# Kernel optimization log

Hardware: AMD Instinct MI355X
Metric: run time of the kernel (lower is better)

The kernel has to match this reference:

```python
import jax, jax.numpy as jnp
import numpy as np

N, D, E, H, TOPK = 16384, 1024, 8, 4096, 2


def setup_inputs() -> dict:
    key = jax.random.key(0)
    ks = jax.random.split(key, 7)
    s_in = 1.0 / np.sqrt(D)
    s_h = 1.0 / np.sqrt(H)
    return {
        "x": jax.random.normal(ks[0], (N, D), jnp.float32),
        "Wg": jax.random.uniform(ks[1], (D, E), jnp.float32, -s_in, s_in),
        "bg": jnp.zeros((E,), jnp.float32),
        "W1": jax.random.uniform(ks[2], (E, D, H), jnp.float32, -s_in, s_in),
        "b1": jax.random.uniform(ks[3], (E, H), jnp.float32, -s_in, s_in),
        "W2": jax.random.uniform(ks[4], (E, H, D), jnp.float32, -s_h, s_h),
        "b2": jax.random.uniform(ks[5], (E, D), jnp.float32, -s_h, s_h),
    }


def _moe_forward(x, Wg, bg, W1, b1, W2, b2):
    # Gate: softmax over experts, top-k, renormalize (standard TopKGate)
    logits = x @ Wg + bg                       # (N, E)
    probs = jax.nn.softmax(logits, axis=-1)
    gates, idxs = jax.lax.top_k(probs, TOPK)   # (N, K)
    gates = gates / jnp.sum(gates, axis=-1, keepdims=True)

    # combine weight per token per expert: cw[n,e] = sum_k gates[n,k]*[idxs[n,k]==e]
    onehot = jax.nn.one_hot(idxs, E, dtype=x.dtype)        # (N, K, E)
    cw = jnp.einsum("nk,nke->ne", gates, onehot)           # (N, E)

    # per-expert 2-layer MLP, gated combine (loop over small fixed expert set)
    out = jnp.zeros_like(x)
    for e in range(E):
        h = jax.nn.relu(x @ W1[e] + b1[e])     # (N, H)
        y = h @ W2[e] + b2[e]                  # (N, D)
        out = out + cw[:, e:e + 1] * y

    # aux loss: for each expert with >=1 routed token, add mean(gates[:,0])^2
    counts = jnp.sum(onehot, axis=(0, 1))                  # (E,)
    active = (counts > 0).astype(x.dtype)                  # (E,)
    m = jnp.mean(gates[:, 0])
    aux_loss = jnp.sum(active) * m * m
    return out, aux_loss


def reference(x, Wg, bg, W1, b1, W2, b2):
    return _moe_forward(x, Wg, bg, W1, b1, W2, b2)
```

## Files before the change

kernel.cpp:

```cpp
#include <hip/hip_runtime.h>
#include <stdint.h>

typedef unsigned short u16;
typedef __bf16 bf16x8 __attribute__((ext_vector_type(8)));
typedef float f32x4 __attribute__((ext_vector_type(4)));

#define N_TOK 16384
#define DIM   1024
#define NEXP  8
#define HID   4096
#define MTILES 264
#define PADROWS 33792

__device__ __forceinline__ u16 f2bf(float f) {
  uint32_t u = __builtin_bit_cast(uint32_t, f);
  u += 0x7fffu + ((u >> 16) & 1u);
  return (u16)(u >> 16);
}

__device__ __forceinline__ float bf2f(u16 v) {
  uint32_t u = (uint32_t)v << 16;
  return __builtin_bit_cast(float, u);
}

__device__ __forceinline__ void gload16(const void* g, void* l) {
  __builtin_amdgcn_global_load_lds(
      (const __attribute__((address_space(1))) uint32_t*)g,
      (__attribute__((address_space(3))) uint32_t*)l, 16, 0, 0);
}


__global__ void k_zero(int* counts) {
  if (threadIdx.x < NEXP) counts[threadIdx.x] = 0;
}

__global__ void k_tcast(const float* __restrict__ src, u16* __restrict__ dst,
                        int R, int C) {
  __shared__ float tile[32][33];
  int nc = C >> 5, nr = R >> 5;
  int t = blockIdx.x;
  int cb = t % nc; t /= nc;
  int rb = t % nr; int ee = t / nr;
  const float* s0 = src + ((size_t)ee * R + (size_t)rb * 32) * C + cb * 32;
  int tx = threadIdx.x & 31, ty = threadIdx.x >> 5;
#pragma unroll
  for (int i = 0; i < 4; ++i)
    tile[ty + i * 8][tx] = s0[(size_t)(ty + i * 8) * C + tx];
  __syncthreads();
  u16* d0 = dst + ((size_t)ee * C + (size_t)cb * 32) * R + rb * 32;
#pragma unroll
  for (int i = 0; i < 4; ++i)
    d0[(size_t)(ty + i * 8) * R + tx] = f2bf(tile[tx][ty + i * 8]);
}


__global__ __launch_bounds__(256) void k_gate(
    const float* __restrict__ x, const float* __restrict__ Wg,
    const float* __restrict__ bg, u16* __restrict__ xb,
    int* __restrict__ tok_e, float* __restrict__ tok_g,
    float* __restrict__ blocksums) {
  __shared__ float wg_s[NEXP * DIM];
  __shared__ float s4[4];
  for (int i = threadIdx.x; i < NEXP * DIM; i += 256) {
    int k = i >> 3, e = i & 7;
    wg_s[e * DIM + k] = Wg[i];
  }
  __syncthreads();
  int lane = threadIdx.x & 63, wv = threadIdx.x >> 6;
  int n = blockIdx.x * 4 + wv;
  const float4* xr4 = (const float4*)(x + (size_t)n * DIM);
  float4 xv[4];
#pragma unroll
  for (int i = 0; i < 4; ++i) xv[i] = xr4[lane + 64 * i];
  ushort4* xo4 = (ushort4*)(xb + (size_t)n * DIM);
#pragma unroll
  for (int i = 0; i < 4; ++i) {
    ushort4 p;
    p.x = f2bf(xv[i].x); p.y = f2bf(xv[i].y);
    p.z = f2bf(xv[i].z); p.w = f2bf(xv[i].w);
    xo4[lane + 64 * i] = p;
  }
  float acc[8];
#pragma unroll
  for (int e = 0; e < 8; ++e) {
    const float4* w4 = (const float4*)(wg_s + e * DIM);
    float a = 0.f;
#pragma unroll
    for (int i = 0; i < 4; ++i) {
      float4 wv4 = w4[lane + 64 * i];
      a += xv[i].x * wv4.x + xv[i].y * wv4.y + xv[i].z * wv4.z +
           xv[i].w * wv4.w;
    }
    acc[e] = a;
  }
#pragma unroll
  for (int e = 0; e < 8; ++e)
#pragma unroll
    for (int off = 32; off > 0; off >>= 1)
      acc[e] += __shfl_xor(acc[e], off);

  if (lane == 0) {
    float l0 = -1e30f, l1 = -1e30f; int e0 = 0, e1 = 0;
#pragma unroll
    for (int e = 0; e < 8; ++e) {
      float v = acc[e] + bg[e];
      if (v > l0) { l1 = l0; e1 = e0; l0 = v; e0 = e; }
      else if (v > l1) { l1 = v; e1 = e; }
    }
    float g0 = 1.f / (1.f + expf(l1 - l0));
    float g1 = 1.f - g0;
    tok_e[2 * n] = e0; tok_e[2 * n + 1] = e1;
    tok_g[2 * n] = g0; tok_g[2 * n + 1] = g1;
    s4[wv] = g0;
  }
  __syncthreads();
  if (threadIdx.x == 0) blocksums[blockIdx.x] = s4[0] + s4[1] + s4[2] + s4[3];
}


__global__ __launch_bounds__(256) void k_hist(const int* __restrict__ tok_e,
                                              int* __restrict__ counts) {
  __shared__ int lcnt[8];
  if (threadIdx.x < 8) lcnt[threadIdx.x] = 0;
  __syncthreads();
  int base4 = (blockIdx.x * 256 + threadIdx.x) * 2;
  const int4* t4 = (const int4*)tok_e;
  int4 a = t4[base4], b = t4[base4 + 1];
  int v[8] = {a.x, a.y, a.z, a.w, b.x, b.y, b.z, b.w};
  int c[8];
#pragma unroll
  for (int ee = 0; ee < 8; ++ee) {
    int s = 0;
#pragma unroll
    for (int i = 0; i < 8; ++i) s += (v[i] == ee);
    c[ee] = s;
  }
  int lane = threadIdx.x & 63;
#pragma unroll
  for (int ee = 0; ee < 8; ++ee) {
    int s = c[ee];
#pragma unroll
    for (int off = 32; off > 0; off >>= 1) s += __shfl_xor(s, off);
    if (lane == 0 && s) atomicAdd(&lcnt[ee], s);
  }
  __syncthreads();
  if (threadIdx.x < 8 && lcnt[threadIdx.x])
    atomicAdd(&counts[threadIdx.x], lcnt[threadIdx.x]);
}


__global__ __launch_bounds__(256) void k_setup(
    const int* __restrict__ counts, const float* __restrict__ blocksums,
    int* __restrict__ padded_off, int* __restrict__ cursor,
    int* __restrict__ row2tok, float* __restrict__ aux_out) {
  __shared__ float red[256];
  __shared__ int off_s[9];
  float s = 0.f;
  for (int i = threadIdx.x; i < 4096; i += 256) s += blocksums[i];
  red[threadIdx.x] = s;
  __syncthreads();
  for (int st = 128; st > 0; st >>= 1) {
    if (threadIdx.x < st) red[threadIdx.x] += red[threadIdx.x + st];
    __syncthreads();
  }
  if (threadIdx.x == 0) {
    int off = 0, nact = 0;
    for (int e = 0; e < 8; ++e) {
      off_s[e] = off;
      int c = counts[e];
      if (c > 0) nact++;
      off += ((c + 127) >> 7) << 7;
      cursor[e] = 0;
    }
    off_s[8] = off;
    for (int e = 0; e <= 8; ++e) padded_off[e] = off_s[e];
    float m = red[0] / (float)N_TOK;
    *aux_out = (float)nact * m * m;
  }
  __syncthreads();
  for (int idx = threadIdx.x; idx < NEXP * 128; idx += 256) {
    int e = idx >> 7, i = idx & 127;
    int slot = off_s[e] + counts[e] + i;
    if (slot < off_s[e + 1]) row2tok[slot] = 0;
  }
}


__global__ __launch_bounds__(256) void k_scatter(
    int* __restrict__ tok_e, const int* __restrict__ padded_off,
    int* __restrict__ cursor, int* __restrict__ row2tok) {
  __shared__ int lcnt[8], lbase[8];
  if (threadIdx.x < 8) lcnt[threadIdx.x] = 0;
  __syncthreads();
  int n = blockIdx.x * 256 + threadIdx.x;
  int e0 = tok_e[2 * n], e1 = tok_e[2 * n + 1];
  int p0 = atomicAdd(&lcnt[e0], 1);
  int p1 = atomicAdd(&lcnt[e1], 1);
  __syncthreads();
  if (threadIdx.x < 8 && lcnt[threadIdx.x])
    lbase[threadIdx.x] = atomicAdd(&cursor[threadIdx.x], lcnt[threadIdx.x]);
  __syncthreads();
  int s0 = padded_off[e0] + lbase[e0] + p0;
  int s1 = padded_off[e1] + lbase[e1] + p1;
  row2tok[s0] = n;
  row2tok[s1] = n;
  tok_e[2 * n] = s0;
  tok_e[2 * n + 1] = s1;
}


template <int KDIM, int MODE, int NTL>
__global__ __launch_bounds__(256, 3) void k_gemm(
    const u16* __restrict__ Asrc, const u16* __restrict__ Wt,
    const float* __restrict__ bias, const int* __restrict__ row2tok,
    const int* __restrict__ padded_off, u16* __restrict__ Out) {
  __shared__ u16 Abuf[3][4096];
  __shared__ u16 Bbuf[3][4096];
  constexpr int NDIM = MODE ? DIM : HID;
  static_assert((1 << NTL) == NDIM / 128, "NT must equal n-tile count");
  int d = blockIdx.x;
  int xcd = d & 7;
  int n_t = (d >> 3) & ((1 << NTL) - 1);
  int rg  = d >> (3 + NTL);
  int row0 = (rg * 8 + xcd) * 128;
  if (row0 >= padded_off[8]) return;
  int e = 0;
  while (row0 >= padded_off[e + 1]) ++e;
  int n0 = n_t * 128;
  int tid = threadIdx.x, lane = tid & 63, wv = tid >> 6;
  int wm = wv >> 1, wn = wv & 1;
  int fr = lane & 15, fq = lane >> 4;
  int ra0 = tid >> 2, ra1 = 64 + (tid >> 2);
  int ca = (((tid & 3) ^ ((tid >> 3) & 3))) * 8;
  const u16 *asrc0, *asrc1;
  if (MODE == 0) {
    asrc0 = Asrc + (size_t)row2tok[row0 + ra0] * KDIM + ca;
    asrc1 = Asrc + (size_t)row2tok[row0 + ra1] * KDIM + ca;
  } else {
    asrc0 = Asrc + (size_t)(row0 + ra0) * KDIM + ca;
    asrc1 = Asrc + (size_t)(row0 + ra1) * KDIM + ca;
  }
  const u16* bb = Wt + (size_t)e * (HID * DIM);
  const u16* bsrc0 = bb + (size_t)(n0 + ra0) * KDIM + ca;
  const u16* bsrc1 = bb + (size_t)(n0 + ra1) * KDIM + ca;
  int lo = wv * 512;
  int sq = (fq ^ ((fr >> 1) & 3)) * 8;

  f32x4 acc[4][4];
#pragma unroll
  for (int i = 0; i < 4; ++i)
#pragma unroll
    for (int j = 0; j < 4; ++j) acc[i][j] = (f32x4){0.f, 0.f, 0.f, 0.f};
  bf16x8 av[4], bv[4];

#define STG(b, kt)                                 \
  do {                                             \
    int ko = (kt) * 32;                            \
    gload16(asrc0 + ko, &Abuf[b][lo]);             \
    gload16(asrc1 + ko, &Abuf[b][2048 + lo]);      \
    gload16(bsrc0 + ko, &Bbuf[b][lo]);             \
    gload16(bsrc1 + ko, &Bbuf[b][2048 + lo]);      \
  } while (0)

#define CMP(b)                                                                 \
  do {                                                                         \
    _Pragma("unroll") for (int fm = 0; fm < 4; ++fm)                           \
        av[fm] = *(const bf16x8*)&Abuf[b][(wm * 64 + fm * 16 + fr) * 32 + sq]; \
    _Pragma("unroll") for (int fn = 0; fn < 4; ++fn)                           \
        bv[fn] = *(const bf16x8*)&Bbuf[b][(wn * 64 + fn * 16 + fr) * 32 + sq]; \
    _Pragma("unroll") for (int fm = 0; fm < 4; ++fm)                           \
        _Pragma("unroll") for (int fn = 0; fn < 4; ++fn)                       \
            acc[fm][fn] = __builtin_amdgcn_mfma_f32_16x16x32_bf16(             \
                av[fm], bv[fn], acc[fm][fn], 0, 0, 0);                         \
  } while (0)

  constexpr int NK = KDIM / 32;
  STG(0, 0);
  STG(1, 1);
  int rb = 0;
  for (int kt = 0; kt < NK - 2; ++kt) {
    int sb = rb + 2; if (sb >= 3) sb -= 3;
    STG(sb, kt + 2);
    asm volatile("s_waitcnt vmcnt(8)" ::: "memory");
    asm volatile("s_barrier" ::: "memory");
    CMP(rb);
    asm volatile("s_waitcnt lgkmcnt(0)" ::: "memory");
    asm volatile("s_barrier" ::: "memory");
    if (++rb == 3) rb = 0;
  }
  asm volatile("s_waitcnt vmcnt(4)" ::: "memory");
  asm volatile("s_barrier" ::: "memory");
  CMP(rb);
  if (++rb == 3) rb = 0;
  asm volatile("s_waitcnt vmcnt(0)" ::: "memory");
  asm volatile("s_barrier" ::: "memory");
  CMP(rb);
#undef STG
#undef CMP

  float bv4[4];
#pragma unroll
  for (int fn = 0; fn < 4; ++fn)
    bv4[fn] = bias[e * NDIM + n0 + wn * 64 + fn * 16 + fr];

#pragma unroll
  for (int fm = 0; fm < 4; ++fm) {
#pragma unroll
    for (int j = 0; j < 4; ++j) {
      int grow = row0 + wm * 64 + fm * 16 + fq * 4 + j;
      u16* orow = Out + (size_t)grow * NDIM + n0 + wn * 64 + fr;
#pragma unroll
      for (int fn = 0; fn < 4; ++fn) {
        float v = acc[fm][fn][j] + bv4[fn];
        if (MODE == 0) v = v > 0.f ? v : 0.f;
        orow[fn * 16] = f2bf(v);
      }
    }
  }
}


__global__ __launch_bounds__(256) void k_combine(
    const u16* __restrict__ y, const int* __restrict__ slots,
    const float* __restrict__ tok_g, float* __restrict__ out) {
  int n = blockIdx.x;
  int s0 = slots[2 * n], s1 = slots[2 * n + 1];
  float g0 = tok_g[2 * n], g1 = tok_g[2 * n + 1];
  int d = threadIdx.x * 4;
  ushort4 a = *(const ushort4*)(y + (size_t)s0 * DIM + d);
  ushort4 b = *(const ushort4*)(y + (size_t)s1 * DIM + d);
  float4 o;
  o.x = g0 * bf2f(a.x) + g1 * bf2f(b.x);
  o.y = g0 * bf2f(a.y) + g1 * bf2f(b.y);
  o.z = g0 * bf2f(a.z) + g1 * bf2f(b.z);
  o.w = g0 * bf2f(a.w) + g1 * bf2f(b.w);
  *(float4*)(out + (size_t)n * DIM + d) = o;
}


extern "C" void kernel_launch(void* const* d_in, const int* in_sizes, int n_in,
                              void* d_out, int out_size, void* d_ws,
                              size_t ws_size, hipStream_t stream) {
  const float* x  = (const float*)d_in[0];
  const float* Wg = (const float*)d_in[1];
  const float* bg = (const float*)d_in[2];
  const float* W1 = (const float*)d_in[3];
  const float* b1 = (const float*)d_in[4];
  const float* W2 = (const float*)d_in[5];
  const float* b2 = (const float*)d_in[6];
  float* out = (float*)d_out;

  char* w = (char*)d_ws;
  u16* xb          = (u16*)(w);
  u16* y           = (u16*)(w);
  u16* w1t         = (u16*)(w + 33554432);
  u16* w2t         = (u16*)(w + 100663296);
  u16* h           = (u16*)(w + 167772160);
  int* tok_e       = (int*)(w + 444596224);
  float* tok_g     = (float*)(w + 444727296);
  int* counts      = (int*)(w + 444858368);
  int* cursor      = (int*)(w + 444858624);
  int* padded_off  = (int*)(w + 444858880);
  int* row2tok     = (int*)(w + 444859136);
  float* blocksums = (float*)(w + 445129472);

  k_zero<<<1, 64, 0, stream>>>(counts);
  k_gate<<<4096, 256, 0, stream>>>(x, Wg, bg, xb, tok_e, tok_g, blocksums);
  k_hist<<<16, 256, 0, stream>>>(tok_e, counts);
  k_setup<<<1, 256, 0, stream>>>(counts, blocksums, padded_off, cursor, row2tok,
                                 out + (size_t)N_TOK * DIM);
  k_scatter<<<64, 256, 0, stream>>>(tok_e, padded_off, cursor, row2tok);
  k_tcast<<<32768, 256, 0, stream>>>(W1, w1t, DIM, HID);
  k_tcast<<<32768, 256, 0, stream>>>(W2, w2t, HID, DIM);
  k_gemm<DIM, 0, 5><<<MTILES * (HID / 128), 256, 0, stream>>>(
      xb, w1t, b1, row2tok, padded_off, h);
  k_gemm<HID, 1, 3><<<MTILES * (DIM / 128), 256, 0, stream>>>(
      h, w2t, b2, row2tok, padded_off, y);
  k_combine<<<N_TOK, 256, 0, stream>>>(y, tok_e, tok_g, out);
}
```

Before: 874.9 us.

## Use 256x256 tiles with 8-wave pipelined schedule for first expert GEMM

Replaces the first expert GEMM with a 512-thread kernel computing 256x256 output tiles, using large LDS buffers with an 8-phase interleaved load/compute schedule, raised wave priority around MFMA bursts, and per-expert padding to 256 rows. This targets higher arithmetic intensity and better overlap of global-to-LDS loads with matrix math in the largest GEMM. The workspace is reorganised so one transposed weight buffer is reused between the two GEMMs, with the output y split across two regions. Larger padding adds wasted rows and the big tile cuts occupancy, and the reordered transposes serialize weight casts with GEMMs.

After: 827.0 us. -5.5%, faster.

```diff
diff --git a/kernel.cpp b/kernel.cpp
--- a/kernel.cpp
+++ b/kernel.cpp
@@ -9,8 +9,9 @@
 #define DIM   1024
 #define NEXP  8
 #define HID   4096
-#define MTILES 264
-#define PADROWS 33792
+#define MT256 136
+#define MT128 272
+#define PADROWS 34816
 
 __device__ __forceinline__ u16 f2bf(float f) {
   uint32_t u = __builtin_bit_cast(uint32_t, f);
@@ -169,7 +170,7 @@
       off_s[e] = off;
       int c = counts[e];
       if (c > 0) nact++;
-      off += ((c + 127) >> 7) << 7;
+      off += ((c + 255) >> 8) << 8;
       cursor[e] = 0;
     }
     off_s[8] = off;
@@ -178,8 +179,8 @@
     *aux_out = (float)nact * m * m;
   }
   __syncthreads();
-  for (int idx = threadIdx.x; idx < NEXP * 128; idx += 256) {
-    int e = idx >> 7, i = idx & 127;
+  for (int idx = threadIdx.x; idx < NEXP * 256; idx += 256) {
+    int e = idx >> 8, i = idx & 255;
     int slot = off_s[e] + counts[e] + i;
     if (slot < off_s[e + 1]) row2tok[slot] = 0;
   }
@@ -209,19 +210,139 @@
 }
 
 
-template <int KDIM, int MODE, int NTL>
-__global__ __launch_bounds__(256, 3) void k_gemm(
-    const u16* __restrict__ Asrc, const u16* __restrict__ Wt,
-    const float* __restrict__ bias, const int* __restrict__ row2tok,
-    const int* __restrict__ padded_off, u16* __restrict__ Out) {
+__global__ __launch_bounds__(512, 2) void k_gemm1_8p(
+    const u16* __restrict__ xb, const u16* __restrict__ w1t,
+    const float* __restrict__ b1, const int* __restrict__ row2tok,
+    const int* __restrict__ padded_off, u16* __restrict__ h) {
+  __shared__ u16 ldsA[32768];
+  __shared__ u16 ldsB[32768];
+  int n0 = blockIdx.x * 256;
+  int row0 = blockIdx.y * 256;
+  if (row0 >= padded_off[8]) return;
+  int e = 0;
+  while (row0 >= padded_off[e + 1]) ++e;
+  int tid = threadIdx.x, lane = tid & 63, wv = tid >> 6;
+  int wm = wv >> 2, wn = wv & 3;
+  int fr = lane & 15, fq = lane >> 4;
+  int r = tid >> 2;
+  int clog = ((tid & 3) ^ ((tid >> 3) & 3)) * 8;
+  const u16* a0 = xb + (size_t)row2tok[row0 + r] * DIM + clog;
+  const u16* a1 = xb + (size_t)row2tok[row0 + 128 + r] * DIM + clog;
+  const u16* wp = w1t + (size_t)e * (HID * DIM);
+  const u16* b0p = wp + (size_t)(n0 + r) * DIM + clog;
+  const u16* b1p = wp + (size_t)(n0 + 128 + r) * DIM + clog;
+
+  f32x4 acc[8][4];
+#pragma unroll
+  for (int i = 0; i < 8; ++i)
+#pragma unroll
+    for (int j = 0; j < 4; ++j) acc[i][j] = (f32x4){0.f, 0.f, 0.f, 0.f};
+  bf16x8 av[4], bv[4];
+
+#define ST1(ISB, T, KK, KOF)                                              \
+  do {                                                                   \
+    u16* d_ = ((ISB) ? ldsB : ldsA) + ((T) * 2 + (KK)) * 8192 + wv * 512; \
+    gload16(((ISB) ? b0p : a0) + (KOF), d_);                             \
+    gload16(((ISB) ? b1p : a1) + (KOF), d_ + 4096);                      \
+  } while (0)
+
+#define RD8(T, KK, IH, LB)                                                \
+  do {                                                                   \
+    const u16* Ar = ldsA + ((T) * 2 + (KK)) * 8192;                      \
+    _Pragma("unroll") for (int i = 0; i < 4; ++i) {                      \
+      int ar = wm * 128 + ((IH) * 4 + i) * 16 + fr;                      \
+      av[i] = *(const bf16x8*)&Ar[ar * 32 + ((fq ^ ((ar >> 1) & 3)) * 8)]; \
+    }                                                                    \
+    if (LB) {                                                            \
+      const u16* Br = ldsB + ((T) * 2 + (KK)) * 8192;                    \
+      _Pragma("unroll") for (int j = 0; j < 4; ++j) {                    \
+        int br = wn * 64 + j * 16 + fr;                                  \
+        bv[j] = *(const bf16x8*)&Br[br * 32 + ((fq ^ ((br >> 1) & 3)) * 8)]; \
+      }                                                                  \
+    }                                                                    \
+  } while (0)
+
+#define PH(T, KK, IH, LB, DOST, SB, STT, SKK, SKOF, VM6, VM0)            \
+  do {                                                                   \
+    RD8(T, KK, IH, LB);                                                  \
+    if (DOST) ST1(SB, STT, SKK, SKOF);                                   \
+    if (VM6) asm volatile("s_waitcnt vmcnt(6)" ::: "memory");            \
+    if (VM0) asm volatile("s_waitcnt vmcnt(0)" ::: "memory");            \
+    asm volatile("s_barrier" ::: "memory");                              \
+    asm volatile("s_waitcnt lgkmcnt(0)" ::: "memory");                   \
+    __builtin_amdgcn_sched_barrier(0);                                   \
+    __builtin_amdgcn_s_setprio(1);                                       \
+    _Pragma("unroll") for (int i = 0; i < 4; ++i)                        \
+      _Pragma("unroll") for (int j = 0; j < 4; ++j)                      \
+        acc[(IH) * 4 + i][j] = __builtin_amdgcn_mfma_f32_16x16x32_bf16(  \
+            av[i], bv[j], acc[(IH) * 4 + i][j], 0, 0, 0);                \
+    __builtin_amdgcn_s_setprio(0);                                       \
+    asm volatile("s_barrier" ::: "memory");                              \
+  } while (0)
+
+  ST1(1, 0, 0, 0);  ST1(0, 0, 0, 0);  ST1(1, 0, 1, 32); ST1(0, 0, 1, 32);
+  ST1(1, 1, 0, 64); ST1(0, 1, 0, 64); ST1(1, 1, 1, 96);
+  asm volatile("s_waitcnt vmcnt(6)" ::: "memory");
+  asm volatile("s_barrier" ::: "memory");
+
+  constexpr int NI = DIM / 128;
+  for (int kt = 0; kt < NI - 1; ++kt) {
+    int k0 = kt * 128;
+    PH(0, 0, 0, 1, 1, 0, 1, 1, k0 + 96,  0, 0);
+    PH(0, 0, 1, 0, 1, 1, 0, 0, k0 + 128, 0, 0);
+    PH(0, 1, 0, 1, 1, 0, 0, 0, k0 + 128, 0, 0);
+    PH(0, 1, 1, 0, 1, 1, 0, 1, k0 + 160, 1, 0);
+    PH(1, 0, 0, 1, 1, 0, 0, 1, k0 + 160, 0, 0);
+    PH(1, 0, 1, 0, 1, 1, 1, 0, k0 + 192, 0, 0);
+    PH(1, 1, 0, 1, 1, 0, 1, 0, k0 + 192, 0, 0);
+    PH(1, 1, 1, 0, 1, 1, 1, 1, k0 + 224, 1, 0);
+  }
+  {
+    int k0 = (NI - 1) * 128;
+    PH(0, 0, 0, 1, 1, 0, 1, 1, k0 + 96, 0, 0);
+    PH(0, 0, 1, 0, 0, 0, 0, 0, 0, 0, 0);
+    PH(0, 1, 0, 1, 0, 0, 0, 0, 0, 0, 0);
+    PH(0, 1, 1, 0, 0, 0, 0, 0, 0, 0, 1);
+    PH(1, 0, 0, 1, 0, 0, 0, 0, 0, 0, 0);
+    PH(1, 0, 1, 0, 0, 0, 0, 0, 0, 0, 0);
+    PH(1, 1, 0, 1, 0, 0, 0, 0, 0, 0, 0);
+    PH(1, 1, 1, 0, 0, 0, 0, 0, 0, 0, 0);
+  }
+#undef PH
+#undef RD8
+#undef ST1
+
+  float bv4[4];
+#pragma unroll
+  for (int j = 0; j < 4; ++j)
+    bv4[j] = b1[e * HID + n0 + wn * 64 + j * 16 + fr];
+
+#pragma unroll
+  for (int rf = 0; rf < 8; ++rf) {
+#pragma unroll
+    for (int jj = 0; jj < 4; ++jj) {
+      int grow = row0 + wm * 128 + rf * 16 + fq * 4 + jj;
+      u16* hr = h + (size_t)grow * HID + n0 + wn * 64 + fr;
+#pragma unroll
+      for (int j = 0; j < 4; ++j) {
+        float v = acc[rf][j][jj] + bv4[j];
+        hr[j * 16] = f2bf(v > 0.f ? v : 0.f);
+      }
+    }
+  }
+}
+
+
+__global__ __launch_bounds__(256, 3) void k_gemm2(
+    const u16* __restrict__ hh, const u16* __restrict__ w2t,
+    const float* __restrict__ b2, const int* __restrict__ padded_off,
+    u16* __restrict__ y0, u16* __restrict__ y1) {
   __shared__ u16 Abuf[3][4096];
   __shared__ u16 Bbuf[3][4096];
-  constexpr int NDIM = MODE ? DIM : HID;
-  static_assert((1 << NTL) == NDIM / 128, "NT must equal n-tile count");
   int d = blockIdx.x;
   int xcd = d & 7;
-  int n_t = (d >> 3) & ((1 << NTL) - 1);
-  int rg  = d >> (3 + NTL);
+  int n_t = (d >> 3) & 7;
+  int rg  = d >> 6;
   int row0 = (rg * 8 + xcd) * 128;
   if (row0 >= padded_off[8]) return;
   int e = 0;
@@ -232,17 +353,11 @@
   int fr = lane & 15, fq = lane >> 4;
   int ra0 = tid >> 2, ra1 = 64 + (tid >> 2);
   int ca = (((tid & 3) ^ ((tid >> 3) & 3))) * 8;
-  const u16 *asrc0, *asrc1;
-  if (MODE == 0) {
-    asrc0 = Asrc + (size_t)row2tok[row0 + ra0] * KDIM + ca;
-    asrc1 = Asrc + (size_t)row2tok[row0 + ra1] * KDIM + ca;
-  } else {
-    asrc0 = Asrc + (size_t)(row0 + ra0) * KDIM + ca;
-    asrc1 = Asrc + (size_t)(row0 + ra1) * KDIM + ca;
-  }
-  const u16* bb = Wt + (size_t)e * (HID * DIM);
-  const u16* bsrc0 = bb + (size_t)(n0 + ra0) * KDIM + ca;
-  const u16* bsrc1 = bb + (size_t)(n0 + ra1) * KDIM + ca;
+  const u16* asrc0 = hh + (size_t)(row0 + ra0) * HID + ca;
+  const u16* asrc1 = hh + (size_t)(row0 + ra1) * HID + ca;
+  const u16* bb = w2t + (size_t)e * (HID * DIM);
+  const u16* bsrc0 = bb + (size_t)(n0 + ra0) * HID + ca;
+  const u16* bsrc1 = bb + (size_t)(n0 + ra1) * HID + ca;
   int lo = wv * 512;
   int sq = (fq ^ ((fr >> 1) & 3)) * 8;
 
@@ -274,7 +389,7 @@
                 av[fm], bv[fn], acc[fm][fn], 0, 0, 0);                         \
   } while (0)
 
-  constexpr int NK = KDIM / 32;
+  constexpr int NK = HID / 32;
   STG(0, 0);
   STG(1, 1);
   int rb = 0;
@@ -301,34 +416,38 @@
   float bv4[4];
 #pragma unroll
   for (int fn = 0; fn < 4; ++fn)
-    bv4[fn] = bias[e * NDIM + n0 + wn * 64 + fn * 16 + fr];
+    bv4[fn] = b2[e * DIM + n0 + wn * 64 + fn * 16 + fr];
 
 #pragma unroll
   for (int fm = 0; fm < 4; ++fm) {
 #pragma unroll
     for (int j = 0; j < 4; ++j) {
       int grow = row0 + wm * 64 + fm * 16 + fq * 4 + j;
-      u16* orow = Out + (size_t)grow * NDIM + n0 + wn * 64 + fr;
-#pragma unroll
-      for (int fn = 0; fn < 4; ++fn) {
-        float v = acc[fm][fn][j] + bv4[fn];
-        if (MODE == 0) v = v > 0.f ? v : 0.f;
-        orow[fn * 16] = f2bf(v);
-      }
+      u16* ybase = grow < 16384 ? y0 + (size_t)grow * DIM
+                                : y1 + (size_t)(grow - 16384) * DIM;
+      u16* orow = ybase + n0 + wn * 64 + fr;
+#pragma unroll
+      for (int fn = 0; fn < 4; ++fn)
+        orow[fn * 16] = f2bf(acc[fm][fn][j] + bv4[fn]);
     }
   }
 }
 
 
 __global__ __launch_bounds__(256) void k_combine(
-    const u16* __restrict__ y, const int* __restrict__ slots,
-    const float* __restrict__ tok_g, float* __restrict__ out) {
+    const u16* __restrict__ y0, const u16* __restrict__ y1,
+    const int* __restrict__ slots, const float* __restrict__ tok_g,
+    float* __restrict__ out) {
   int n = blockIdx.x;
   int s0 = slots[2 * n], s1 = slots[2 * n + 1];
   float g0 = tok_g[2 * n], g1 = tok_g[2 * n + 1];
   int d = threadIdx.x * 4;
-  ushort4 a = *(const ushort4*)(y + (size_t)s0 * DIM + d);
-  ushort4 b = *(const ushort4*)(y + (size_t)s1 * DIM + d);
+  const u16* ya = (s0 < 16384 ? y0 + (size_t)s0 * DIM
+                              : y1 + (size_t)(s0 - 16384) * DIM) + d;
+  const u16* yb = (s1 < 16384 ? y0 + (size_t)s1 * DIM
+                              : y1 + (size_t)(s1 - 16384) * DIM) + d;
+  ushort4 a = *(const ushort4*)ya;
+  ushort4 b = *(const ushort4*)yb;
   float4 o;
   o.x = g0 * bf2f(a.x) + g1 * bf2f(b.x);
   o.y = g0 * bf2f(a.y) + g1 * bf2f(b.y);
@@ -352,17 +471,17 @@
 
   char* w = (char*)d_ws;
   u16* xb          = (u16*)(w);
-  u16* y           = (u16*)(w);
-  u16* w1t         = (u16*)(w + 33554432);
-  u16* w2t         = (u16*)(w + 100663296);
-  u16* h           = (u16*)(w + 167772160);
-  int* tok_e       = (int*)(w + 444596224);
-  float* tok_g     = (float*)(w + 444727296);
-  int* counts      = (int*)(w + 444858368);
-  int* cursor      = (int*)(w + 444858624);
-  int* padded_off  = (int*)(w + 444858880);
-  int* row2tok     = (int*)(w + 444859136);
-  float* blocksums = (float*)(w + 445129472);
+  u16* y0          = (u16*)(w);
+  u16* wT          = (u16*)(w + 33554432);
+  u16* h           = (u16*)(w + 100663296);
+  u16* y1          = (u16*)(w + 385875968);
+  int* tok_e       = (int*)(w + 423624704);
+  float* tok_g     = (float*)(w + 423755776);
+  int* counts      = (int*)(w + 423886848);
+  int* cursor      = (int*)(w + 423887104);
+  int* padded_off  = (int*)(w + 423887360);
+  int* row2tok     = (int*)(w + 423887616);
+  float* blocksums = (float*)(w + 424026880);
 
   k_zero<<<1, 64, 0, stream>>>(counts);
   k_gate<<<4096, 256, 0, stream>>>(x, Wg, bg, xb, tok_e, tok_g, blocksums);
@@ -370,11 +489,11 @@
   k_setup<<<1, 256, 0, stream>>>(counts, blocksums, padded_off, cursor, row2tok,
                                  out + (size_t)N_TOK * DIM);
   k_scatter<<<64, 256, 0, stream>>>(tok_e, padded_off, cursor, row2tok);
-  k_tcast<<<32768, 256, 0, stream>>>(W1, w1t, DIM, HID);
-  k_tcast<<<32768, 256, 0, stream>>>(W2, w2t, HID, DIM);
-  k_gemm<DIM, 0, 5><<<MTILES * (HID / 128), 256, 0, stream>>>(
-      xb, w1t, b1, row2tok, padded_off, h);
-  k_gemm<HID, 1, 3><<<MTILES * (DIM / 128), 256, 0, stream>>>(
-      h, w2t, b2, row2tok, padded_off, y);
-  k_combine<<<N_TOK, 256, 0, stream>>>(y, tok_e, tok_g, out);
-}
+  k_tcast<<<32768, 256, 0, stream>>>(W1, wT, DIM, HID);
+  k_gemm1_8p<<<dim3(HID / 256, MT256), 512, 0, stream>>>(
+      xb, wT, b1, row2tok, padded_off, h);
+  k_tcast<<<32768, 256, 0, stream>>>(W2, wT, HID, DIM);
+  k_gemm2<<<MT128 * (DIM / 128), 256, 0, stream>>>(
+      h, wT, b2, padded_off, y0, y1);
+  k_combine<<<N_TOK, 256, 0, stream>>>(y0, y1, tok_e, tok_g, out);
+}
```
